# Optimization experiments

Measured on AMD Instinct MI355X. Metric: run time of the kernel, lower is better.

Reference implementation:

```python
import jax, jax.numpy as jnp
import numpy as np

B, CIN, N, E = 8192, 16, 96, 768
NF, EMB, NCLS = 64, 128, 210


def _p(key, shape, scale=0.05):
    return jax.random.normal(key, shape, dtype=jnp.float32) * scale


def setup_inputs() -> dict:
    key = jax.random.key(0)
    ks = jax.random.split(key, 20)
    return {
        "src": jax.random.normal(ks[0], (B, CIN, N), dtype=jnp.float32),
        "edge_index": jax.random.randint(ks[1], (2, E), 0, N, dtype=jnp.int32),
        "gcn1_w": _p(ks[2], (CIN, 64)), "gcn1_b": _p(ks[3], (64,)),
        "gcn2_w": _p(ks[4], (64, 32)), "gcn2_b": _p(ks[5], (32,)),
        "conv1_w": _p(ks[6], (NF, 32, 7)), "conv1_b": _p(ks[7], (NF,)),
        "conv2_w": _p(ks[8], (NF * 2, NF, 5)), "conv2_b": _p(ks[9], (NF * 2,)),
        "conv3_w": _p(ks[10], (NF * 4, NF * 2, 3)), "conv3_b": _p(ks[11], (NF * 4,)),
        "fc1_w": _p(ks[12], (3072, EMB)), "fc1_b": _p(ks[13], (EMB,)),
        "cls1_w": _p(ks[14], (EMB, EMB)), "cls1_b": _p(ks[15], (EMB,)),
        "cls2_w": _p(ks[16], (EMB, NCLS)), "cls2_b": _p(ks[17], (NCLS,)),
    }


def gcn_conv(x, edge_index, W, b):
    n = x.shape[1]
    loops = jnp.arange(n, dtype=edge_index.dtype)
    row = jnp.concatenate([edge_index[0], loops])  # targets
    col = jnp.concatenate([edge_index[1], loops])  # sources
    deg = jnp.zeros((n,), x.dtype).at[row].add(1.0)
    dinv = jax.lax.rsqrt(jnp.maximum(deg, 1e-12))
    norm = dinv[row] * dinv[col]                 # [E+N]
    h = x @ W                                    # [B, N, Fout]
    msgs = h[:, col, :] * norm[None, :, None]    # gather along node dim
    out = jnp.zeros_like(h).at[:, row, :].add(msgs)  # scatter-add
    return out + b


def conv1d(x, w, b, stride, pad):
    # x: [B, C, L], w: [O, C, K]
    y = jax.lax.conv_general_dilated(x, w, (stride,), [(pad, pad)],
                                     dimension_numbers=("NCH", "OIH", "NCH"))
    return y + b[None, :, None]


def reference(src, edge_index, gcn1_w, gcn1_b, gcn2_w, gcn2_b,
              conv1_w, conv1_b, conv2_w, conv2_b, conv3_w, conv3_b,
              fc1_w, fc1_b, cls1_w, cls1_b, cls2_w, cls2_b):
    x = jnp.transpose(src, (0, 2, 1))            # [B, N, CIN]
    x = jax.nn.relu(gcn_conv(x, edge_index, gcn1_w, gcn1_b))
    x = jax.nn.relu(gcn_conv(x, edge_index, gcn2_w, gcn2_b))
    x = jnp.transpose(x, (0, 2, 1))              # [B, 32, N]
    x = jax.nn.relu(conv1d(x, conv1_w, conv1_b, 2, 3))
    x = jax.nn.relu(conv1d(x, conv2_w, conv2_b, 2, 2))
    x = jax.nn.relu(conv1d(x, conv3_w, conv3_b, 2, 1))
    x = x.reshape(x.shape[0], -1)                # [B, 3072]
    feat = x @ fc1_w + fc1_b
    x = jax.nn.relu(feat)
    x = jax.nn.relu(x @ cls1_w + cls1_b)
    x = x @ cls2_w + cls2_b
    return (x, feat)
```

## Files before the change

### kernel.cpp

```cpp
#include <hip/hip_runtime.h>


typedef __attribute__((ext_vector_type(8))) short short8v;
typedef __attribute__((ext_vector_type(4))) float floatx4;

#define N_NODE 96
#define E_TOT  864
#define BATCH  8192ull

#define R0_OFF   0ull
#define R1_OFF   25165824ull
#define FR_OFF   50331648ull
#define R2_OFF   51380224ull
#define WT_OFF   52428800ull
#define W1N_OFF  (WT_OFF + 0)
#define W2N_OFF  (WT_OFF + 2048)
#define WC1_OFF  (WT_OFF + 4096)
#define WC2_OFF  (WT_OFF + 18432)
#define WC3_OFF  (WT_OFF + 59392)
#define WF1_OFF  (WT_OFF + 157696)
#define WL1_OFF  (WT_OFF + 550912)
#define WL2_OFF  (WT_OFF + 567296)
#define AH_OFF   (WT_OFF + 600064)

__device__ __forceinline__ unsigned short f2b(float f) {
    unsigned int u = __builtin_bit_cast(unsigned int, f);
    u += 0x7fffu + ((u >> 16) & 1u);
    return (unsigned short)(u >> 16);
}
__device__ __forceinline__ float b2f(unsigned short h) {
    unsigned int u = ((unsigned int)h) << 16;
    return __builtin_bit_cast(float, u);
}

__global__ void prep_edges(const int* __restrict__ eidx, unsigned short* __restrict__ adense) {
    __shared__ int rowv[E_TOT];
    __shared__ int colv[E_TOT];
    __shared__ int degi[N_NODE];
    __shared__ float dinv[N_NODE];
    __shared__ float ad[96 * 96];
    const int tid = threadIdx.x;
    for (int e = tid; e < E_TOT; e += 256) {
        int r, c;
        if (e < 768) { r = eidx[e]; c = eidx[768 + e]; }
        else         { r = e - 768; c = r; }
        rowv[e] = r; colv[e] = c;
    }
    for (int n = tid; n < N_NODE; n += 256) degi[n] = 0;
    for (int i = tid; i < 9216; i += 256) ad[i] = 0.f;
    __syncthreads();
    for (int e = tid; e < E_TOT; e += 256) atomicAdd(&degi[rowv[e]], 1);
    __syncthreads();
    for (int n = tid; n < N_NODE; n += 256)
        dinv[n] = rsqrtf(fmaxf((float)degi[n], 1e-12f));
    __syncthreads();
    for (int e = tid; e < E_TOT; e += 256)
        atomicAdd(&ad[rowv[e] * 96 + colv[e]], dinv[rowv[e]] * dinv[colv[e]]);
    __syncthreads();
    for (int i = tid; i < 9216; i += 256) adense[i] = f2b(ad[i]);
}

__global__ void prep_weights(const float* __restrict__ g1w, const float* __restrict__ g2w,
                             const float* __restrict__ w1, const float* __restrict__ w2,
                             const float* __restrict__ w3, const float* __restrict__ f1,
                             const float* __restrict__ l1, const float* __restrict__ l2,
                             unsigned short* __restrict__ wt) {
    long idx = (long)blockIdx.x * 256 + threadIdx.x;
    if (idx >= 600064) return;
    float v;
    if (idx < 2048) {
        int o = idx >> 5, c = idx & 31;
        v = (c < 16) ? g1w[c * 64 + o] : 0.f;
    } else if (idx < 4096) {
        long j = idx - 2048; int g = j >> 6, c = j & 63;
        v = g2w[c * 32 + g];
    } else {
        long base, KS;
        int region;
        if      (idx < 18432)  { base = 4096;   KS = 7;  region = 0; }
        else if (idx < 59392)  { base = 18432;  KS = 10; region = 1; }
        else if (idx < 157696) { base = 59392;  KS = 12; region = 2; }
        else if (idx < 550912) { base = 157696; KS = 96; region = 3; }
        else if (idx < 567296) { base = 550912; KS = 4;  region = 4; }
        else                   { base = 567296; KS = 4;  region = 5; }
        long local = idx - base;
        long g  = local / (KS * 512);
        long rm = local % (KS * 512);
        long ks = rm / 512;
        int lane = (int)((rm % 512) / 8);
        int j    = (int)(rm % 8);
        int quad = lane >> 4, n16 = lane & 15;
        int n = (int)(g * 16 + n16);
        int k = (int)(ks * 32 + quad * 8 + j);
        switch (region) {
            case 0: { int t = k / 32,  c = k % 32;  v = w1[n * 224 + c * 7 + t]; } break;
            case 1: { int t = k / 64,  c = k % 64;  v = w2[n * 320 + c * 5 + t]; } break;
            case 2: { int t = k / 128, c = k % 128; v = w3[n * 384 + c * 3 + t]; } break;
            case 3: { int t = k / 256, o = k % 256; v = f1[(o * 12 + t) * 128 + n]; } break;
            case 4: v = l1[k * 128 + n]; break;
            default: v = (n < 210) ? l2[k * 210 + n] : 0.f; break;
        }
    }
    wt[idx] = f2b(v);
}

__launch_bounds__(256)
__global__ void trans16(const float* __restrict__ src, unsigned short* __restrict__ xt) {
    __shared__ __align__(16) float xs[8 * 1544];
    const int tid = threadIdx.x;
    const int b0 = blockIdx.x * 8;
    for (int u = tid; u < 3072; u += 256) {
        int bl = u / 384, j = u % 384;
        *(float4*)&xs[bl * 1544 + j * 4] =
            *(const float4*)&src[((size_t)(b0 + bl)) * 1536 + j * 4];
    }
    __syncthreads();
    for (int u = tid; u < 768; u += 256) {
        int n = u >> 3, bl = u & 7;
        const float* base = &xs[bl * 1544 + n];
        unsigned int d[8];
#pragma unroll
        for (int c2 = 0; c2 < 8; c2++)
            d[c2] = (unsigned int)f2b(base[(2 * c2) * 96]) |
                    ((unsigned int)f2b(base[(2 * c2 + 1) * 96]) << 16);
        unsigned int* o = (unsigned int*)(xt + ((size_t)n * BATCH + b0 + bl) * 16);
        *(uint4*)&o[0] = make_uint4(d[0], d[1], d[2], d[3]);
        *(uint4*)&o[4] = make_uint4(d[4], d[5], d[6], d[7]);
    }
}

template<int CH, bool RELU>
__launch_bounds__(256)
__global__ void agg_mm(const unsigned short* __restrict__ in,
                       const unsigned short* __restrict__ adense,
                       const float* __restrict__ bias,
                       unsigned short* __restrict__ outp) {
    const size_t NCOL = 8192ull * CH;
    __shared__ __align__(16) unsigned short Al[96 * 104];
    __shared__ __align__(16) unsigned short Bs[96 * 264];
    const int tid = threadIdx.x;
    const size_t c0 = (size_t)blockIdx.x * 256;
    const int w = tid >> 6, lane = tid & 63, quad = lane >> 4, m16 = lane & 15;

    for (int u = tid; u < 1152; u += 256) {
        int r = u / 12, q = u % 12;
        *(short8v*)&Al[r * 104 + q * 8] = *(const short8v*)&adense[r * 96 + q * 8];
    }
    for (int u = tid; u < 3072; u += 256) {
        int r = u >> 5, q = u & 31;
        *(uint4*)&Bs[r * 264 + q * 8] = *(const uint4*)&in[(size_t)r * NCOL + c0 + q * 8];
    }
    __syncthreads();

    floatx4 acc[6][4] = {};
    const int nb = w * 64;
#pragma unroll
    for (int kk = 0; kk < 96; kk += 32) {
        short8v bfr[4];
#pragma unroll
        for (int fn = 0; fn < 4; fn++) {
            const int col = nb + fn * 16 + m16;
#pragma unroll
            for (int j = 0; j < 8; j++)
                bfr[fn][j] = (short)Bs[(kk + quad * 8 + j) * 264 + col];
        }
#pragma unroll
        for (int fm = 0; fm < 6; fm++) {
            short8v afr = *(short8v*)&Al[(fm * 16 + m16) * 104 + kk + quad * 8];
#pragma unroll
            for (int fn = 0; fn < 4; fn++)
                acc[fm][fn] = __builtin_amdgcn_mfma_f32_16x16x32_bf16(afr, bfr[fn], acc[fm][fn], 0, 0, 0);
        }
    }

#pragma unroll
    for (int fm = 0; fm < 6; fm++) {
#pragma unroll
        for (int fn = 0; fn < 4; fn++) {
            const int col = nb + fn * 16 + m16;
            float bv = 0.f;
            if constexpr (RELU) bv = bias[col & (CH - 1)];
#pragma unroll
            for (int r = 0; r < 4; r++) {
                int node = fm * 16 + quad * 4 + r;
                float v = acc[fm][fn][r];
                if constexpr (RELU) v = fmaxf(v + bv, 0.f);
                outp[(size_t)node * NCOL + c0 + col] = f2b(v);
            }
        }
    }
}

__launch_bounds__(256)
__global__ void gcn12(const unsigned short* __restrict__ xa,
                      const unsigned short* __restrict__ w1n,
                      const unsigned short* __restrict__ w2n,
                      const float* __restrict__ b1, unsigned short* __restrict__ hw2) {
    __shared__ __align__(16) unsigned short As[128 * 40];
    __shared__ __align__(16) unsigned short B1s[64 * 40];
    __shared__ __align__(16) unsigned short H1s[128 * 72];
    __shared__ __align__(16) unsigned short B2s[32 * 72];
    const int tid = threadIdx.x;
    const size_t b0 = blockIdx.x * 128;
    const int l = blockIdx.z;
    const int w = tid >> 6, lane = tid & 63, quad = lane >> 4, m16 = lane & 15;

    short8v zz = {0, 0, 0, 0, 0, 0, 0, 0};
    for (int u = tid; u < 512; u += 256) {
        int r = u >> 2, cc = u & 3;
        *(short8v*)&As[r * 40 + cc * 8] = (cc < 2)
            ? *(const short8v*)&xa[((size_t)l * BATCH + b0 + r) * 16 + cc * 8]
            : zz;
    }
    for (int u = tid; u < 256; u += 256) {
        int r = u >> 2, cc = u & 3;
        *(short8v*)&B1s[r * 40 + cc * 8] = *(const short8v*)&w1n[r * 32 + cc * 8];
    }
    for (int u = tid; u < 256; u += 256) {
        int r = u >> 3, cc = u & 7;
        *(short8v*)&B2s[r * 72 + cc * 8] = *(const short8v*)&w2n[r * 64 + cc * 8];
    }
    __syncthreads();

    {
        const int wm = w >> 1, wq = w & 1;
        const int mbase = wm * 64, nbase = wq * 32;
        floatx4 acc[4][2] = {};
#pragma unroll
        for (int fn = 0; fn < 2; fn++) {
            short8v bfr = *(short8v*)&B1s[(nbase + fn * 16 + m16) * 40 + quad * 8];
#pragma unroll
            for (int fm = 0; fm < 4; fm++) {
                short8v afr = *(short8v*)&As[(mbase + fm * 16 + m16) * 40 + quad * 8];
                acc[fm][fn] = __builtin_amdgcn_mfma_f32_16x16x32_bf16(afr, bfr, acc[fm][fn], 0, 0, 0);
            }
        }
        float bv0 = b1[nbase + m16], bv1 = b1[nbase + 16 + m16];
#pragma unroll
        for (int fm = 0; fm < 4; fm++)
#pragma unroll
            for (int r = 0; r < 4; r++) {
                int row = mbase + fm * 16 + quad * 4 + r;
                H1s[row * 72 + nbase + m16]      = f2b(fmaxf(acc[fm][0][r] + bv0, 0.f));
                H1s[row * 72 + nbase + 16 + m16] = f2b(fmaxf(acc[fm][1][r] + bv1, 0.f));
            }
    }
    __syncthreads();

    {
        const int mb2 = w * 32;
        floatx4 acc[2][2] = {};
#pragma unroll
        for (int kk = 0; kk < 64; kk += 32)
#pragma unroll
            for (int fn = 0; fn < 2; fn++) {
                short8v bfr = *(short8v*)&B2s[(fn * 16 + m16) * 72 + kk + quad * 8];
#pragma unroll
                for (int fm = 0; fm < 2; fm++) {
                    short8v afr = *(short8v*)&H1s[(mb2 + fm * 16 + m16) * 72 + kk + quad * 8];
                    acc[fm][fn] = __builtin_amdgcn_mfma_f32_16x16x32_bf16(afr, bfr, acc[fm][fn], 0, 0, 0);
                }
            }
        unsigned short* Cs = As;
#pragma unroll
        for (int fm = 0; fm < 2; fm++)
#pragma unroll
            for (int r = 0; r < 4; r++) {
                int row = mb2 + fm * 16 + quad * 4 + r;
                Cs[row * 40 + m16]      = f2b(acc[fm][0][r]);
                Cs[row * 40 + 16 + m16] = f2b(acc[fm][1][r]);
            }
    }
    __syncthreads();
    for (int u = tid; u < 512; u += 256) {
        int r = u >> 2, cc = u & 3;
        *(short8v*)&hw2[((size_t)l * BATCH + b0 + r) * 32 + cc * 8] =
            *(short8v*)&As[r * 40 + cc * 8];
    }
}

template<int WM, int FN, int NTAP, int CIN, int NOUT, int STRIDE, int PAD, int LIN, int BK, int MODE>
__launch_bounds__(256)
__global__ void gemm_slab(const unsigned short* __restrict__ in,
                          const unsigned short* __restrict__ wn,
                          const float* __restrict__ bias,
                          unsigned short* __restrict__ outb,
                          float* __restrict__ outf) {
    constexpr int BM  = WM * 32;
    constexpr int BN  = FN * 32;
    constexpr int BKP = BK + 8;
    constexpr int CPT = CIN / BK;
    constexpr int NC  = NTAP * CPT;
    constexpr int KS  = NTAP * CIN / 32;
    constexpr int NV  = BM * BK / 8 / 256;
    constexpr int RPV = 256 / (BK / 8);
    constexpr int SZ1 = 2 * BM * BKP;
    constexpr int SZ2 = (MODE == 4) ? 16 : BM * (BN + 8);
    constexpr int POOL = SZ1 > SZ2 ? SZ1 : SZ2;
    __shared__ __align__(16) unsigned short pool[POOL];
    const int tid = threadIdx.x;
    const size_t b0 = blockIdx.x * BM;
    const int n0 = blockIdx.y * BN;
    const int l  = blockIdx.z;
    const int w = tid >> 6, lane = tid & 63, quad = lane >> 4, m16 = lane & 15;
    const int wm = w >> 1, wq = w & 1;
    const int mbase = wm * (WM * 16), nbase = wq * (FN * 16);
    const int gw = (n0 + nbase) >> 4;
    const int lr = tid / (BK / 8);
    const int lc = tid % (BK / 8);
    floatx4 acc[WM][FN] = {};
    const short8v zz8 = {0, 0, 0, 0, 0, 0, 0, 0};

    short8v pre[NV], nxt[NV];
    {
        int pos = STRIDE * l - PAD;
        if (pos >= 0 && pos < LIN) {
            const unsigned short* ag = in + ((size_t)pos * BATCH + b0) * CIN;
#pragma unroll
            for (int v = 0; v < NV; v++)
                pre[v] = *(const short8v*)&ag[(size_t)(lr + v * RPV) * CIN + lc * 8];
        } else {
#pragma unroll
            for (int v = 0; v < NV; v++) pre[v] = zz8;
        }
#pragma unroll
        for (int v = 0; v < NV; v++)
            *(short8v*)&pool[(lr + v * RPV) * BKP + lc * 8] = pre[v];
    }
    int p = 0;
#pragma unroll
    for (int ch = 0; ch < NC; ++ch) {
        __syncthreads();
        if (ch + 1 < NC) {
            int t = (ch + 1) / CPT, inner = (ch + 1) % CPT;
            int pos = STRIDE * l + t - PAD;
            if (pos >= 0 && pos < LIN) {
                const unsigned short* ag = in + ((size_t)pos * BATCH + b0) * CIN + inner * BK;
#pragma unroll
                for (int v = 0; v < NV; v++)
                    nxt[v] = *(const short8v*)&ag[(size_t)(lr + v * RPV) * CIN + lc * 8];
            } else {
#pragma unroll
                for (int v = 0; v < NV; v++) nxt[v] = zz8;
            }
        }
        const unsigned short* As = pool + p * BM * BKP;
        const int kbase = (ch / CPT) * CIN + (ch % CPT) * BK;
#pragma unroll
        for (int kk = 0; kk < BK; kk += 32) {
            const int ksG = (kbase + kk) >> 5;
            short8v bfr[FN];
#pragma unroll
            for (int fn = 0; fn < FN; fn++)
                bfr[fn] = *(const short8v*)&wn[(((size_t)(gw + fn) * KS + ksG) << 9) + lane * 8];
#pragma unroll
            for (int fm = 0; fm < WM; fm++) {
                short8v afr = *(const short8v*)&As[(mbase + fm * 16 + m16) * BKP + kk + quad * 8];
#pragma unroll
                for (int fn = 0; fn < FN; fn++)
                    acc[fm][fn] = __builtin_amdgcn_mfma_f32_16x16x32_bf16(afr, bfr[fn], acc[fm][fn], 0, 0, 0);
            }
        }
        if (ch + 1 < NC) {
            unsigned short* Ad = pool + (p ^ 1) * BM * BKP;
#pragma unroll
            for (int v = 0; v < NV; v++)
                *(short8v*)&Ad[(lr + v * RPV) * BKP + lc * 8] = nxt[v];
        }
        p ^= 1;
    }

    if constexpr (MODE == 4) {
#pragma unroll
        for (int fn = 0; fn < FN; fn++) {
            int cg = n0 + nbase + fn * 16 + m16;
            float bv = (cg < 210) ? bias[cg] : 0.f;
            if (cg < 210) {
#pragma unroll
                for (int fm = 0; fm < WM; fm++)
#pragma unroll
                    for (int r = 0; r < 4; r++) {
                        size_t row = b0 + mbase + fm * 16 + quad * 4 + r;
                        outf[row * 210 + cg] = acc[fm][fn][r] + bv;
                    }
            }
        }
    } else {
        float bv[FN];
#pragma unroll
        for (int fn = 0; fn < FN; fn++) bv[fn] = bias[n0 + nbase + fn * 16 + m16];
        __syncthreads();
        unsigned short* Cs = pool;
#pragma unroll
        for (int fm = 0; fm < WM; fm++)
#pragma unroll
            for (int r = 0; r < 4; r++) {
                int row = mbase + fm * 16 + quad * 4 + r;
#pragma unroll
                for (int fn = 0; fn < FN; fn++)
                    Cs[row * (BN + 8) + nbase + fn * 16 + m16] =
                        f2b(fmaxf(acc[fm][fn][r] + bv[fn], 0.f));
            }
        __syncthreads();
        for (int u = tid; u < BM * (BN / 8); u += 256) {
            int r = u / (BN / 8), cc = u % (BN / 8);
            *(short8v*)&outb[((size_t)l * BATCH + b0 + r) * NOUT + n0 + cc * 8] =
                *(short8v*)&Cs[r * (BN + 8) + cc * 8];
        }
    }
}

__launch_bounds__(256)
__global__ void fc1_splitk(const unsigned short* __restrict__ c3,
                           const unsigned short* __restrict__ wf1,
                           float* __restrict__ part) {
    __shared__ __align__(16) unsigned short pool[2 * 128 * 72];
    const int tid = threadIdx.x;
    const size_t b0 = blockIdx.x * 128;
    const int kg = blockIdx.z;
    const int w = tid >> 6, lane = tid & 63, quad = lane >> 4, m16 = lane & 15;
    const int wm = w >> 1, wq = w & 1;
    const int mbase = wm * 64, nbase = wq * 64;
    const int gw = nbase >> 4;
    const int lr = tid >> 3, lc = tid & 7;
    floatx4 acc[4][4] = {};
    short8v pre[4], nxt[4];

    {
        const unsigned short* ag = c3 + ((size_t)(kg * 2) * BATCH + b0) * 256;
#pragma unroll
        for (int v = 0; v < 4; v++)
            pre[v] = *(const short8v*)&ag[(size_t)(lr + v * 32) * 256 + lc * 8];
#pragma unroll
        for (int v = 0; v < 4; v++)
            *(short8v*)&pool[(lr + v * 32) * 72 + lc * 8] = pre[v];
    }
    int p = 0;
#pragma unroll
    for (int s = 0; s < 8; ++s) {
        __syncthreads();
        if (s + 1 < 8) {
            int t = kg * 2 + ((s + 1) >> 2), inner = (s + 1) & 3;
            const unsigned short* ag = c3 + ((size_t)t * BATCH + b0) * 256 + inner * 64;
#pragma unroll
            for (int v = 0; v < 4; v++)
                nxt[v] = *(const short8v*)&ag[(size_t)(lr + v * 32) * 256 + lc * 8];
        }
        const unsigned short* As = pool + p * 128 * 72;
        const int kbase = (kg * 2 + (s >> 2)) * 256 + (s & 3) * 64;
#pragma unroll
        for (int kk = 0; kk < 64; kk += 32) {
            const int ksG = (kbase + kk) >> 5;
            short8v bfr[4];
#pragma unroll
            for (int fn = 0; fn < 4; fn++)
                bfr[fn] = *(const short8v*)&wf1[(((size_t)(gw + fn) * 96 + ksG) << 9) + lane * 8];
#pragma unroll
            for (int fm = 0; fm < 4; fm++) {
                short8v afr = *(const short8v*)&As[(mbase + fm * 16 + m16) * 72 + kk + quad * 8];
#pragma unroll
                for (int fn = 0; fn < 4; fn++)
                    acc[fm][fn] = __builtin_amdgcn_mfma_f32_16x16x32_bf16(afr, bfr[fn], acc[fm][fn], 0, 0, 0);
            }
        }
        if (s + 1 < 8) {
            unsigned short* Ad = pool + (p ^ 1) * 128 * 72;
#pragma unroll
            for (int v = 0; v < 4; v++)
                *(short8v*)&Ad[(lr + v * 32) * 72 + lc * 8] = nxt[v];
        }
        p ^= 1;
    }
    float* pg = part + (size_t)kg * BATCH * 128;
#pragma unroll
    for (int fm = 0; fm < 4; fm++)
#pragma unroll
        for (int r = 0; r < 4; r++) {
            size_t row = b0 + mbase + fm * 16 + quad * 4 + r;
#pragma unroll
            for (int fn = 0; fn < 4; fn++)
                pg[row * 128 + nbase + fn * 16 + m16] = acc[fm][fn][r];
        }
}

__launch_bounds__(256)
__global__ void fc1_reduce(const float* __restrict__ part, const float* __restrict__ bias,
                           float* __restrict__ feat, unsigned short* __restrict__ fr) {
    const size_t idx = (size_t)blockIdx.x * 256 + threadIdx.x;
    const size_t row = idx >> 5;
    const int    c4  = (int)(idx & 31);
    float4 s = *(const float4*)&bias[c4 * 4];
#pragma unroll
    for (int z = 0; z < 6; z++) {
        float4 p = *(const float4*)&part[(z * BATCH + row) * 128 + c4 * 4];
        s.x += p.x; s.y += p.y; s.z += p.z; s.w += p.w;
    }
    *(float4*)&feat[row * 128 + c4 * 4] = s;
    unsigned int d0 = (unsigned int)f2b(fmaxf(s.x, 0.f)) |
                      ((unsigned int)f2b(fmaxf(s.y, 0.f)) << 16);
    unsigned int d1 = (unsigned int)f2b(fmaxf(s.z, 0.f)) |
                      ((unsigned int)f2b(fmaxf(s.w, 0.f)) << 16);
    *(uint2*)&fr[row * 128 + c4 * 4] = make_uint2(d0, d1);
}

extern "C" void kernel_launch(void* const* d_in, const int* in_sizes, int n_in,
                              void* d_out, int out_size, void* d_ws, size_t ws_size,
                              hipStream_t stream) {
    const float* src  = (const float*)d_in[0];
    const int*   eidx = (const int*)  d_in[1];
    const float* g1w  = (const float*)d_in[2];
    const float* g1b  = (const float*)d_in[3];
    const float* g2w  = (const float*)d_in[4];
    const float* g2b  = (const float*)d_in[5];
    const float* cv1w = (const float*)d_in[6];
    const float* cv1b = (const float*)d_in[7];
    const float* cv2w = (const float*)d_in[8];
    const float* cv2b = (const float*)d_in[9];
    const float* cv3w = (const float*)d_in[10];
    const float* cv3b = (const float*)d_in[11];
    const float* fc1w = (const float*)d_in[12];
    const float* fc1b = (const float*)d_in[13];
    const float* cl1w = (const float*)d_in[14];
    const float* cl1b = (const float*)d_in[15];
    const float* cl2w = (const float*)d_in[16];
    const float* cl2b = (const float*)d_in[17];

    unsigned short* ws16 = (unsigned short*)d_ws;
    float* wsF = (float*)d_ws;
    float* out = (float*)d_out;

    unsigned short* xt  = ws16 + R1_OFF;
    unsigned short* xa  = ws16 + R0_OFF;
    unsigned short* hw2 = ws16 + R1_OFF;
    unsigned short* h2  = ws16 + R0_OFF;
    unsigned short* c1  = ws16 + R1_OFF;
    unsigned short* c2  = ws16 + R0_OFF;
    unsigned short* c3  = ws16 + R1_OFF;
    float*          part = wsF;
    unsigned short* fr  = ws16 + FR_OFF;
    unsigned short* r2  = ws16 + R2_OFF;
    unsigned short* w1n = ws16 + W1N_OFF;
    unsigned short* w2n = ws16 + W2N_OFF;
    unsigned short* wc1 = ws16 + WC1_OFF;
    unsigned short* wc2 = ws16 + WC2_OFF;
    unsigned short* wc3 = ws16 + WC3_OFF;
    unsigned short* wf1 = ws16 + WF1_OFF;
    unsigned short* wl1 = ws16 + WL1_OFF;
    unsigned short* wl2 = ws16 + WL2_OFF;
    unsigned short* ah  = ws16 + AH_OFF;

    float* feat_out = out + 8192ull * 210ull;

    prep_edges<<<1, 256, 0, stream>>>(eidx, ah);
    prep_weights<<<2345, 256, 0, stream>>>(g1w, g2w, cv1w, cv2w, cv3w, fc1w, cl1w, cl2w,
                                           ws16 + WT_OFF);
    trans16<<<1024, 256, 0, stream>>>(src, xt);
    agg_mm<16, false><<<512, 256, 0, stream>>>(xt, ah, nullptr, xa);
    gcn12<<<dim3(64, 1, 96), 256, 0, stream>>>(xa, w1n, w2n, g1b, hw2);
    agg_mm<32, true><<<1024, 256, 0, stream>>>(hw2, ah, g2b, h2);
    gemm_slab<8, 2, 7, 32, 64, 2, 3, 96, 32, 0>
        <<<dim3(32, 1, 48), 256, 0, stream>>>(h2, wc1, cv1b, c1, nullptr);
    gemm_slab<4, 4, 5, 64, 128, 2, 2, 48, 64, 0>
        <<<dim3(64, 1, 24), 256, 0, stream>>>(c1, wc2, cv2b, c2, nullptr);
    gemm_slab<4, 4, 3, 128, 256, 2, 1, 24, 64, 0>
        <<<dim3(64, 2, 12), 256, 0, stream>>>(c2, wc3, cv3b, c3, nullptr);
    fc1_splitk<<<dim3(64, 1, 6), 256, 0, stream>>>(c3, wf1, part);
    fc1_reduce<<<1024, 256, 0, stream>>>(part, fc1b, feat_out, fr);
    gemm_slab<2, 2, 1, 128, 128, 1, 0, 1, 64, 0>
        <<<dim3(128, 2, 1), 256, 0, stream>>>(fr, wl1, cl1b, r2, nullptr);
    gemm_slab<2, 2, 1, 128, 256, 1, 0, 1, 64, 4>
        <<<dim3(128, 4, 1), 256, 0, stream>>>(r2, wl2, cl2b, nullptr, out);
}
```

Measured before the change: 335.8 us.

## Fuse GCN transpose, aggregation and both GCN layers into one kernel

Replaces the transpose kernel, the two dense-adjacency aggregation GEMMs and the per-node GCN weight kernel with a single kernel. Each block owns 4 batch samples and keeps every intermediate (transposed input, aggregated features, H1, HW2) in shared memory, so large intermediate tensors no longer round-trip through global memory. The two prep kernels are also merged into one launch, with block 0 building the adjacency. The cost is a big shared-memory footprint (about 78 KB per block), which limits occupancy, plus small-batch tiles that give less MFMA reuse per load.

```diff
diff --git a/kernel.cpp b/kernel.cpp
--- a/kernel.cpp
+++ b/kernel.cpp
@@ -33,39 +33,41 @@
     return __builtin_bit_cast(float, u);
 }
 
-__global__ void prep_edges(const int* __restrict__ eidx, unsigned short* __restrict__ adense) {
+__global__ void prep_all(const int* __restrict__ eidx,
+                         const float* __restrict__ g1w, const float* __restrict__ g2w,
+                         const float* __restrict__ w1, const float* __restrict__ w2,
+                         const float* __restrict__ w3, const float* __restrict__ f1,
+                         const float* __restrict__ l1, const float* __restrict__ l2,
+                         unsigned short* __restrict__ wt,
+                         unsigned short* __restrict__ adense) {
     __shared__ int rowv[E_TOT];
     __shared__ int colv[E_TOT];
     __shared__ int degi[N_NODE];
     __shared__ float dinv[N_NODE];
     __shared__ float ad[96 * 96];
     const int tid = threadIdx.x;
-    for (int e = tid; e < E_TOT; e += 256) {
-        int r, c;
-        if (e < 768) { r = eidx[e]; c = eidx[768 + e]; }
-        else         { r = e - 768; c = r; }
-        rowv[e] = r; colv[e] = c;
-    }
-    for (int n = tid; n < N_NODE; n += 256) degi[n] = 0;
-    for (int i = tid; i < 9216; i += 256) ad[i] = 0.f;
-    __syncthreads();
-    for (int e = tid; e < E_TOT; e += 256) atomicAdd(&degi[rowv[e]], 1);
-    __syncthreads();
-    for (int n = tid; n < N_NODE; n += 256)
-        dinv[n] = rsqrtf(fmaxf((float)degi[n], 1e-12f));
-    __syncthreads();
-    for (int e = tid; e < E_TOT; e += 256)
-        atomicAdd(&ad[rowv[e] * 96 + colv[e]], dinv[rowv[e]] * dinv[colv[e]]);
-    __syncthreads();
-    for (int i = tid; i < 9216; i += 256) adense[i] = f2b(ad[i]);
-}
-
-__global__ void prep_weights(const float* __restrict__ g1w, const float* __restrict__ g2w,
-                             const float* __restrict__ w1, const float* __restrict__ w2,
-                             const float* __restrict__ w3, const float* __restrict__ f1,
-                             const float* __restrict__ l1, const float* __restrict__ l2,
-                             unsigned short* __restrict__ wt) {
-    long idx = (long)blockIdx.x * 256 + threadIdx.x;
+    if (blockIdx.x == 0) {
+        for (int e = tid; e < E_TOT; e += 256) {
+            int r, c;
+            if (e < 768) { r = eidx[e]; c = eidx[768 + e]; }
+            else         { r = e - 768; c = r; }
+            rowv[e] = r; colv[e] = c;
+        }
+        for (int n = tid; n < N_NODE; n += 256) degi[n] = 0;
+        for (int i = tid; i < 9216; i += 256) ad[i] = 0.f;
+        __syncthreads();
+        for (int e = tid; e < E_TOT; e += 256) atomicAdd(&degi[rowv[e]], 1);
+        __syncthreads();
+        for (int n = tid; n < N_NODE; n += 256)
+            dinv[n] = rsqrtf(fmaxf((float)degi[n], 1e-12f));
+        __syncthreads();
+        for (int e = tid; e < E_TOT; e += 256)
+            atomicAdd(&ad[rowv[e] * 96 + colv[e]], dinv[rowv[e]] * dinv[colv[e]]);
+        __syncthreads();
+        for (int i = tid; i < 9216; i += 256) adense[i] = f2b(ad[i]);
+        return;
+    }
+    long idx = (long)(blockIdx.x - 1) * 256 + tid;
     if (idx >= 600064) return;
     float v;
     if (idx < 2048) {
@@ -105,177 +107,158 @@
 }
 
 __launch_bounds__(256)
-__global__ void trans16(const float* __restrict__ src, unsigned short* __restrict__ xt) {
-    __shared__ __align__(16) float xs[8 * 1544];
+__global__ void gcn_fused(const float* __restrict__ src,
+                          const unsigned short* __restrict__ adense,
+                          const unsigned short* __restrict__ w1n,
+                          const unsigned short* __restrict__ w2n,
+                          const float* __restrict__ b1,
+                          const float* __restrict__ b2,
+                          unsigned short* __restrict__ h2) {
+    __shared__ __align__(16) unsigned short pool[39936];
+    float* FLT = (float*)pool;
+    unsigned short* AH2  = pool;
+    unsigned short* HW2T = pool;
+    unsigned short* Xt   = pool + 13312;
+    unsigned short* AH5  = pool + 13312;
+    unsigned short* XA   = pool + 19968;
+    unsigned short* H1S  = pool + 35328;
+
     const int tid = threadIdx.x;
-    const int b0 = blockIdx.x * 8;
-    for (int u = tid; u < 3072; u += 256) {
+    const int w = tid >> 6, lane = tid & 63, quad = lane >> 4, m16 = lane & 15;
+    const size_t b0 = (size_t)blockIdx.x * 4;
+
+    short8v w1f[4], w2f[2][2];
+    float bv1[4], bv2[2];
+#pragma unroll
+    for (int fn = 0; fn < 4; fn++) {
+        w1f[fn] = *(const short8v*)&w1n[(fn * 16 + m16) * 32 + quad * 8];
+        bv1[fn] = b1[fn * 16 + m16];
+    }
+#pragma unroll
+    for (int fn = 0; fn < 2; fn++) {
+#pragma unroll
+        for (int kk = 0; kk < 2; kk++)
+            w2f[fn][kk] = *(const short8v*)&w2n[(fn * 16 + m16) * 64 + kk * 32 + quad * 8];
+        bv2[fn] = b2[fn * 16 + m16];
+    }
+
+    for (int u = tid; u < 1536; u += 256) {
         int bl = u / 384, j = u % 384;
-        *(float4*)&xs[bl * 1544 + j * 4] =
-            *(const float4*)&src[((size_t)(b0 + bl)) * 1536 + j * 4];
+        *(float4*)&FLT[bl * 1544 + j * 4] = *(const float4*)&src[(b0 + bl) * 1536 + j * 4];
+    }
+    {
+        short8v z = {0, 0, 0, 0, 0, 0, 0, 0};
+        for (int u = tid; u < 768; u += 256)
+            *(short8v*)&XA[(u >> 1) * 40 + 16 + (u & 1) * 8] = z;
     }
     __syncthreads();
+
     for (int u = tid; u < 768; u += 256) {
-        int n = u >> 3, bl = u & 7;
-        const float* base = &xs[bl * 1544 + n];
-        unsigned int d[8];
-#pragma unroll
-        for (int c2 = 0; c2 < 8; c2++)
-            d[c2] = (unsigned int)f2b(base[(2 * c2) * 96]) |
-                    ((unsigned int)f2b(base[(2 * c2 + 1) * 96]) << 16);
-        unsigned int* o = (unsigned int*)(xt + ((size_t)n * BATCH + b0 + bl) * 16);
-        *(uint4*)&o[0] = make_uint4(d[0], d[1], d[2], d[3]);
-        *(uint4*)&o[4] = make_uint4(d[4], d[5], d[6], d[7]);
-    }
-}
-
-template<int CH, bool RELU>
-__launch_bounds__(256)
-__global__ void agg_mm(const unsigned short* __restrict__ in,
-                       const unsigned short* __restrict__ adense,
-                       const float* __restrict__ bias,
-                       unsigned short* __restrict__ outp) {
-    const size_t NCOL = 8192ull * CH;
-    __shared__ __align__(16) unsigned short Al[96 * 104];
-    __shared__ __align__(16) unsigned short Bs[96 * 264];
-    const int tid = threadIdx.x;
-    const size_t c0 = (size_t)blockIdx.x * 256;
-    const int w = tid >> 6, lane = tid & 63, quad = lane >> 4, m16 = lane & 15;
+        int col = u / 12, seg = u % 12;
+        int bl = col >> 4, c = col & 15;
+        const float* f = &FLT[bl * 1544 + c * 96 + seg * 8];
+        unsigned int d[4];
+#pragma unroll
+        for (int i = 0; i < 4; i++)
+            d[i] = (unsigned int)f2b(f[2 * i]) | ((unsigned int)f2b(f[2 * i + 1]) << 16);
+        *(uint4*)&Xt[col * 104 + seg * 8] = make_uint4(d[0], d[1], d[2], d[3]);
+    }
+    __syncthreads();
 
     for (int u = tid; u < 1152; u += 256) {
         int r = u / 12, q = u % 12;
-        *(short8v*)&Al[r * 104 + q * 8] = *(const short8v*)&adense[r * 96 + q * 8];
-    }
-    for (int u = tid; u < 3072; u += 256) {
-        int r = u >> 5, q = u & 31;
-        *(uint4*)&Bs[r * 264 + q * 8] = *(const uint4*)&in[(size_t)r * NCOL + c0 + q * 8];
+        *(short8v*)&AH2[r * 104 + q * 8] = *(const short8v*)&adense[r * 96 + q * 8];
     }
     __syncthreads();
 
-    floatx4 acc[6][4] = {};
-    const int nb = w * 64;
-#pragma unroll
-    for (int kk = 0; kk < 96; kk += 32) {
-        short8v bfr[4];
-#pragma unroll
-        for (int fn = 0; fn < 4; fn++) {
-            const int col = nb + fn * 16 + m16;
-#pragma unroll
-            for (int j = 0; j < 8; j++)
-                bfr[fn][j] = (short)Bs[(kk + quad * 8 + j) * 264 + col];
-        }
-#pragma unroll
-        for (int fm = 0; fm < 6; fm++) {
-            short8v afr = *(short8v*)&Al[(fm * 16 + m16) * 104 + kk + quad * 8];
-#pragma unroll
-            for (int fn = 0; fn < 4; fn++)
-                acc[fm][fn] = __builtin_amdgcn_mfma_f32_16x16x32_bf16(afr, bfr[fn], acc[fm][fn], 0, 0, 0);
-        }
-    }
-
-#pragma unroll
-    for (int fm = 0; fm < 6; fm++) {
-#pragma unroll
-        for (int fn = 0; fn < 4; fn++) {
-            const int col = nb + fn * 16 + m16;
-            float bv = 0.f;
-            if constexpr (RELU) bv = bias[col & (CH - 1)];
+    {
+        floatx4 acc[6] = {};
+#pragma unroll
+        for (int kk = 0; kk < 96; kk += 32) {
+            short8v bfr = *(const short8v*)&Xt[(w * 16 + m16) * 104 + kk + quad * 8];
+#pragma unroll
+            for (int fm = 0; fm < 6; fm++) {
+                short8v afr = *(const short8v*)&AH2[(fm * 16 + m16) * 104 + kk + quad * 8];
+                acc[fm] = __builtin_amdgcn_mfma_f32_16x16x32_bf16(afr, bfr, acc[fm], 0, 0, 0);
+            }
+        }
+#pragma unroll
+        for (int fm = 0; fm < 6; fm++)
 #pragma unroll
             for (int r = 0; r < 4; r++) {
                 int node = fm * 16 + quad * 4 + r;
-                float v = acc[fm][fn][r];
-                if constexpr (RELU) v = fmaxf(v + bv, 0.f);
-                outp[(size_t)node * NCOL + c0 + col] = f2b(v);
-            }
-        }
-    }
-}
-
-__launch_bounds__(256)
-__global__ void gcn12(const unsigned short* __restrict__ xa,
-                      const unsigned short* __restrict__ w1n,
-                      const unsigned short* __restrict__ w2n,
-                      const float* __restrict__ b1, unsigned short* __restrict__ hw2) {
-    __shared__ __align__(16) unsigned short As[128 * 40];
-    __shared__ __align__(16) unsigned short B1s[64 * 40];
-    __shared__ __align__(16) unsigned short H1s[128 * 72];
-    __shared__ __align__(16) unsigned short B2s[32 * 72];
-    const int tid = threadIdx.x;
-    const size_t b0 = blockIdx.x * 128;
-    const int l = blockIdx.z;
-    const int w = tid >> 6, lane = tid & 63, quad = lane >> 4, m16 = lane & 15;
-
-    short8v zz = {0, 0, 0, 0, 0, 0, 0, 0};
-    for (int u = tid; u < 512; u += 256) {
-        int r = u >> 2, cc = u & 3;
-        *(short8v*)&As[r * 40 + cc * 8] = (cc < 2)
-            ? *(const short8v*)&xa[((size_t)l * BATCH + b0 + r) * 16 + cc * 8]
-            : zz;
-    }
-    for (int u = tid; u < 256; u += 256) {
-        int r = u >> 2, cc = u & 3;
-        *(short8v*)&B1s[r * 40 + cc * 8] = *(const short8v*)&w1n[r * 32 + cc * 8];
-    }
-    for (int u = tid; u < 256; u += 256) {
-        int r = u >> 3, cc = u & 7;
-        *(short8v*)&B2s[r * 72 + cc * 8] = *(const short8v*)&w2n[r * 64 + cc * 8];
+                XA[(node * 4 + w) * 40 + m16] = f2b(acc[fm][r]);
+            }
     }
     __syncthreads();
 
+    unsigned short* H1W = H1S + w * 1152;
+    for (int cc = 0; cc < 6; cc++) {
+        const int rowbase = w * 96 + cc * 16;
+        short8v afr1 = *(const short8v*)&XA[(rowbase + m16) * 40 + quad * 8];
+        floatx4 a1[4];
+#pragma unroll
+        for (int fn = 0; fn < 4; fn++) {
+            floatx4 zc = {0.f, 0.f, 0.f, 0.f};
+            a1[fn] = __builtin_amdgcn_mfma_f32_16x16x32_bf16(afr1, w1f[fn], zc, 0, 0, 0);
+        }
+#pragma unroll
+        for (int fn = 0; fn < 4; fn++)
+#pragma unroll
+            for (int r = 0; r < 4; r++)
+                H1W[(quad * 4 + r) * 72 + fn * 16 + m16] =
+                    f2b(fmaxf(a1[fn][r] + bv1[fn], 0.f));
+        floatx4 a2[2] = {};
+#pragma unroll
+        for (int kk = 0; kk < 2; kk++) {
+            short8v afr2 = *(const short8v*)&H1W[m16 * 72 + kk * 32 + quad * 8];
+#pragma unroll
+            for (int fn = 0; fn < 2; fn++)
+                a2[fn] = __builtin_amdgcn_mfma_f32_16x16x32_bf16(afr2, w2f[fn][kk], a2[fn], 0, 0, 0);
+        }
+#pragma unroll
+        for (int fn = 0; fn < 2; fn++)
+#pragma unroll
+            for (int r = 0; r < 4; r++) {
+                int row = rowbase + quad * 4 + r;
+                int node = row >> 2, bl = row & 3;
+                HW2T[(bl * 32 + fn * 16 + m16) * 104 + node] = f2b(a2[fn][r]);
+            }
+    }
+    __syncthreads();
+
+    for (int u = tid; u < 1152; u += 256) {
+        int r = u / 12, q = u % 12;
+        *(short8v*)&AH5[r * 104 + q * 8] = *(const short8v*)&adense[r * 96 + q * 8];
+    }
+    __syncthreads();
+
     {
-        const int wm = w >> 1, wq = w & 1;
-        const int mbase = wm * 64, nbase = wq * 32;
-        floatx4 acc[4][2] = {};
-#pragma unroll
-        for (int fn = 0; fn < 2; fn++) {
-            short8v bfr = *(short8v*)&B1s[(nbase + fn * 16 + m16) * 40 + quad * 8];
-#pragma unroll
-            for (int fm = 0; fm < 4; fm++) {
-                short8v afr = *(short8v*)&As[(mbase + fm * 16 + m16) * 40 + quad * 8];
-                acc[fm][fn] = __builtin_amdgcn_mfma_f32_16x16x32_bf16(afr, bfr, acc[fm][fn], 0, 0, 0);
-            }
-        }
-        float bv0 = b1[nbase + m16], bv1 = b1[nbase + 16 + m16];
-#pragma unroll
-        for (int fm = 0; fm < 4; fm++)
-#pragma unroll
-            for (int r = 0; r < 4; r++) {
-                int row = mbase + fm * 16 + quad * 4 + r;
-                H1s[row * 72 + nbase + m16]      = f2b(fmaxf(acc[fm][0][r] + bv0, 0.f));
-                H1s[row * 72 + nbase + 16 + m16] = f2b(fmaxf(acc[fm][1][r] + bv1, 0.f));
-            }
-    }
-    __syncthreads();
-
-    {
-        const int mb2 = w * 32;
-        floatx4 acc[2][2] = {};
-#pragma unroll
-        for (int kk = 0; kk < 64; kk += 32)
-#pragma unroll
-            for (int fn = 0; fn < 2; fn++) {
-                short8v bfr = *(short8v*)&B2s[(fn * 16 + m16) * 72 + kk + quad * 8];
-#pragma unroll
-                for (int fm = 0; fm < 2; fm++) {
-                    short8v afr = *(short8v*)&H1s[(mb2 + fm * 16 + m16) * 72 + kk + quad * 8];
-                    acc[fm][fn] = __builtin_amdgcn_mfma_f32_16x16x32_bf16(afr, bfr, acc[fm][fn], 0, 0, 0);
+        floatx4 acc[6][2] = {};
+#pragma unroll
+        for (int kk = 0; kk < 96; kk += 32) {
+            short8v bfr[2];
+#pragma unroll
+            for (int fn = 0; fn < 2; fn++)
+                bfr[fn] = *(const short8v*)&HW2T[(w * 32 + fn * 16 + m16) * 104 + kk + quad * 8];
+#pragma unroll
+            for (int fm = 0; fm < 6; fm++) {
+                short8v afr = *(const short8v*)&AH5[(fm * 16 + m16) * 104 + kk + quad * 8];
+#pragma unroll
+                for (int fn = 0; fn < 2; fn++)
+                    acc[fm][fn] = __builtin_amdgcn_mfma_f32_16x16x32_bf16(afr, bfr[fn], acc[fm][fn], 0, 0, 0);
+            }
+        }
+#pragma unroll
+        for (int fm = 0; fm < 6; fm++)
+#pragma unroll
+            for (int fn = 0; fn < 2; fn++)
+#pragma unroll
+                for (int r = 0; r < 4; r++) {
+                    int node = fm * 16 + quad * 4 + r;
+                    h2[((size_t)node * BATCH + b0 + w) * 32 + fn * 16 + m16] =
+                        f2b(fmaxf(acc[fm][fn][r] + bv2[fn], 0.f));
                 }
-            }
-        unsigned short* Cs = As;
-#pragma unroll
-        for (int fm = 0; fm < 2; fm++)
-#pragma unroll
-            for (int r = 0; r < 4; r++) {
-                int row = mb2 + fm * 16 + quad * 4 + r;
-                Cs[row * 40 + m16]      = f2b(acc[fm][0][r]);
-                Cs[row * 40 + 16 + m16] = f2b(acc[fm][1][r]);
-            }
-    }
-    __syncthreads();
-    for (int u = tid; u < 512; u += 256) {
-        int r = u >> 2, cc = u & 3;
-        *(short8v*)&hw2[((size_t)l * BATCH + b0 + r) * 32 + cc * 8] =
-            *(short8v*)&As[r * 40 + cc * 8];
     }
 }
 
@@ -529,9 +512,6 @@
     float* wsF = (float*)d_ws;
     float* out = (float*)d_out;
 
-    unsigned short* xt  = ws16 + R1_OFF;
-    unsigned short* xa  = ws16 + R0_OFF;
-    unsigned short* hw2 = ws16 + R1_OFF;
     unsigned short* h2  = ws16 + R0_OFF;
     unsigned short* c1  = ws16 + R1_OFF;
     unsigned short* c2  = ws16 + R0_OFF;
@@ -551,13 +531,9 @@
 
     float* feat_out = out + 8192ull * 210ull;
 
-    prep_edges<<<1, 256, 0, stream>>>(eidx, ah);
-    prep_weights<<<2345, 256, 0, stream>>>(g1w, g2w, cv1w, cv2w, cv3w, fc1w, cl1w, cl2w,
-                                           ws16 + WT_OFF);
-    trans16<<<1024, 256, 0, stream>>>(src, xt);
-    agg_mm<16, false><<<512, 256, 0, stream>>>(xt, ah, nullptr, xa);
-    gcn12<<<dim3(64, 1, 96), 256, 0, stream>>>(xa, w1n, w2n, g1b, hw2);
-    agg_mm<32, true><<<1024, 256, 0, stream>>>(hw2, ah, g2b, h2);
+    prep_all<<<2346, 256, 0, stream>>>(eidx, g1w, g2w, cv1w, cv2w, cv3w, fc1w, cl1w, cl2w,
+                                       ws16 + WT_OFF, ah);
+    gcn_fused<<<2048, 256, 0, stream>>>(src, ah, w1n, w2n, g1b, g2b, h2);
     gemm_slab<8, 2, 7, 32, 64, 2, 3, 96, 32, 0>
         <<<dim3(32, 1, 48), 256, 0, stream>>>(h2, wc1, cv1b, c1, nullptr);
     gemm_slab<4, 4, 5, 64, 128, 2, 2, 48, 64, 0>
```

After: 297.1 us. 11.5% less time.
